# Kernel tuning notes

Hardware: AMD Instinct MI355X
Metric: run time of the kernel (lower is better)

## Reference

```python
import jax, jax.numpy as jnp
import numpy as np

B, C, H, W = 16, 256, 64, 64
K, HID, ITERS, EPS = 4, 512, 3, 1e-8


def _ln(x, g, b, eps=1e-5):
    m = jnp.mean(x, axis=-1, keepdims=True)
    v = jnp.mean((x - m) ** 2, axis=-1, keepdims=True)
    return (x - m) * jax.lax.rsqrt(v + eps) * g + b


def setup_inputs() -> dict:
    key = jax.random.key(0)
    ks = jax.random.split(key, 24)

    def lin(k, o, i):
        lim = np.sqrt(6.0 / (o + i)).astype(np.float32)
        return jax.random.uniform(k, (o, i), jnp.float32, -lim, lim)

    return {
        "x": jax.random.normal(ks[0], (B, C, H, W), jnp.float32),
        "noise": jax.random.normal(ks[1], (B, K, C), jnp.float32),
        "slot_mu": jax.random.normal(ks[2], (1, 1, C), jnp.float32),
        "slot_log_sigma": jnp.zeros((1, 1, C), jnp.float32),
        "ln_in_g": jnp.ones((C,)), "ln_in_b": jnp.zeros((C,)),
        "ln_sl_g": jnp.ones((C,)), "ln_sl_b": jnp.zeros((C,)),
        "ln_mlp_g": jnp.ones((C,)), "ln_mlp_b": jnp.zeros((C,)),
        "Wq": lin(ks[3], C, C), "bq": jnp.zeros((C,)),
        "Wk": lin(ks[4], C, C), "bk": jnp.zeros((C,)),
        "Wv": lin(ks[5], C, C), "bv": jnp.zeros((C,)),
        "Wu": lin(ks[6], C, 2 * C), "bu": jnp.zeros((C,)),
        "W1": lin(ks[7], HID, C), "b1": jnp.zeros((HID,)),
        "W2": lin(ks[8], C, HID), "b2": jnp.zeros((C,)),
        "We1": lin(ks[9], C // 2, C), "be1": jnp.zeros((C // 2,)),
        "We2": lin(ks[10], 1, C // 2), "be2": jnp.zeros((1,)),
    }


def reference(x, noise, slot_mu, slot_log_sigma, ln_in_g, ln_in_b, ln_sl_g, ln_sl_b,
              ln_mlp_g, ln_mlp_b, Wq, bq, Wk, bk, Wv, bv, Wu, bu, W1, b1, W2, b2,
              We1, be1, We2, be2):
    # b c h w -> b (h w) c
    xn = x.reshape(B, C, H * W).transpose(0, 2, 1)
    xn = _ln(xn, ln_in_g, ln_in_b)
    # k, v depend only on xn; hoisted out of the loop (same math)
    k = jnp.einsum('bnc,dc->bnd', xn, Wk) + bk
    v = jnp.einsum('bnc,dc->bnd', xn, Wv) + bv
    scale = C ** (-0.5)
    slots = slot_mu + jnp.exp(slot_log_sigma) * noise
    for _ in range(ITERS):
        prev = slots
        s = _ln(slots, ln_sl_g, ln_sl_b)
        q = jnp.einsum('bkc,dc->bkd', s, Wq) + bq
        attn = jax.nn.softmax(jnp.einsum('bkc,bnc->bkn', q, k) * scale, axis=1)
        w = attn / (jnp.sum(attn, axis=-1, keepdims=True) + EPS)
        updates = jnp.einsum('bkn,bnc->bkc', w, v)
        combined = jnp.concatenate([prev, updates], axis=-1)  # (B,K,2C)
        slots = jnp.einsum('bkc,dc->bkd', combined, Wu) + bu + prev
        m = _ln(slots, ln_mlp_g, ln_mlp_b)
        h = jax.nn.gelu(jnp.einsum('bkc,hc->bkh', m, W1) + b1, approximate=False)
        slots = slots + jnp.einsum('bkh,ch->bkc', h, W2) + b2
    e = jax.nn.gelu(jnp.einsum('bkc,dc->bkd', slots, We1) + be1, approximate=False)
    slot_weights = jax.nn.sigmoid(jnp.einsum('bkd,od->bko', e, We2) + be2)[..., 0]
    return slots, slot_weights
```

## Files before the change

### kernel.cpp

```cpp
#include <hip/hip_runtime.h>
#include <math.h>

#define B_    16
#define C_    256
#define NPIX  4096
#define K_    4
#define HID_  512
#define ITERS_ 3
#define NROWS (B_*NPIX)
#define EPS_  1e-8f

__device__ __forceinline__ float gelu_f(float x) {
    return 0.5f * x * (1.0f + erff(x * 0.70710678118654752f));
}

__device__ __forceinline__ unsigned short f2bf(float x) {
    union { float f; unsigned u; } v; v.f = x;
    unsigned r = v.u + 0x7fffu + ((v.u >> 16) & 1u);
    return (unsigned short)(r >> 16);
}
__device__ __forceinline__ float bflo(unsigned u) {
    union { unsigned u; float f; } v; v.u = u << 16; return v.f;
}
__device__ __forceinline__ float bfhi(unsigned u) {
    union { unsigned u; float f; } v; v.u = u & 0xffff0000u; return v.f;
}
__device__ __forceinline__ float4 shfl_xor4(float4 v, int m) {
    v.x = __shfl_xor(v.x, m); v.y = __shfl_xor(v.y, m);
    v.z = __shfl_xor(v.z, m); v.w = __shfl_xor(v.w, m);
    return v;
}
__device__ __forceinline__ void fma4(float4& a, const float4 w, const float4 s) {
    a.x = fmaf(w.x, s.x, a.x); a.y = fmaf(w.y, s.y, a.y);
    a.z = fmaf(w.z, s.z, a.z); a.w = fmaf(w.w, s.w, a.w);
}
__device__ __forceinline__ float hsum4(const float4 a) {
    return (a.x + a.y) + (a.z + a.w);
}

__device__ __forceinline__ void redpair256t(float a, float b, int t, float* r8,
                                            float& o1, float& o2) {
    #pragma unroll
    for (int m = 1; m <= 32; m <<= 1) { a += __shfl_xor(a, m); b += __shfl_xor(b, m); }
    if ((t & 63) == 0) { r8[(t >> 6) * 2] = a; r8[(t >> 6) * 2 + 1] = b; }
    __syncthreads();
    o1 = r8[0] + r8[2] + r8[4] + r8[6];
    o2 = r8[1] + r8[3] + r8[5] + r8[7];
}

__global__ __launch_bounds__(256) void prep_pack_kernel(
    const float* __restrict__ Wu, const float* __restrict__ W1,
    const float* __restrict__ W2, const float* __restrict__ We1,
    const float* __restrict__ Wq, const float* __restrict__ bk,
    const float* __restrict__ bq,
    float4* __restrict__ WuC4, float4* __restrict__ W14,
    float4* __restrict__ W24, float4* __restrict__ We14,
    float* __restrict__ wqoff) {
    __shared__ float r4[4];
    int i = blockIdx.x * 256 + threadIdx.x;
    if (blockIdx.x == 352) {
        int c = threadIdx.x;
        float s = 0.f;
        for (int dd = 0; dd < 256; ++dd) s = fmaf(Wq[dd * 256 + c], bk[dd], s);
        wqoff[c] = s;
        float p = bq[c] * bk[c];
        #pragma unroll
        for (int m = 1; m <= 32; m <<= 1) p += __shfl_xor(p, m);
        if ((c & 63) == 0) r4[c >> 6] = p;
        __syncthreads();
        if (c == 0) wqoff[256] = r4[0] + r4[1] + r4[2] + r4[3];
        return;
    }
    if (i < 16384) {
        int c4 = i >> 8, dd = i & 255;
        WuC4[i] = *(const float4*)&Wu[dd * 512 + c4 * 4];
    } else if (i < 49152) {
        int j = i - 16384; int c4 = j >> 9, h = j & 511;
        W14[j] = *(const float4*)&W1[h * 256 + c4 * 4];
    } else if (i < 81920) {
        int j = i - 49152; int h4 = j >> 8, dd = j & 255;
        W24[j] = *(const float4*)&W2[dd * 512 + h4 * 4];
    } else {
        int j = i - 81920; int c4 = j >> 7, e = j & 127;
        We14[j] = *(const float4*)&We1[e * 256 + c4 * 4];
    }
}

__global__ __launch_bounds__(256) void prep_compose_kernel(
    const float* __restrict__ Wu, const float* __restrict__ Wv,
    const float* __restrict__ Wk, const float* __restrict__ Wq,
    const float* __restrict__ bv, const float* __restrict__ bq,
    float4* __restrict__ WuC4, float4* __restrict__ Wqk4,
    float* __restrict__ bv2, float* __restrict__ bqk) {
    __shared__ float wur[256], wkc[256];
    __shared__ float ldsA[256], ldsB[256];
    __shared__ float r1[4], r2[4];
    const int d = blockIdx.x, c = threadIdx.x;
    wur[c] = Wu[d * 512 + 256 + c];
    wkc[c] = Wk[c * 256 + d];
    __syncthreads();
    float a = 0.f, b = 0.f;
    #pragma unroll 4
    for (int e = 0; e < 256; ++e) {
        a = fmaf(wur[e], Wv[e * 256 + c], a);
        b = fmaf(wkc[e], Wq[e * 256 + c], b);
    }
    ldsA[c] = a; ldsB[c] = b;
    float p1 = wur[c] * bv[c], p2 = wkc[c] * bq[c];
    #pragma unroll
    for (int m = 1; m <= 32; m <<= 1) { p1 += __shfl_xor(p1, m); p2 += __shfl_xor(p2, m); }
    if ((c & 63) == 0) { r1[c >> 6] = p1; r2[c >> 6] = p2; }
    __syncthreads();
    if (c < 64) {
        float4 qa = { ldsA[4 * c], ldsA[4 * c + 1], ldsA[4 * c + 2], ldsA[4 * c + 3] };
        float4 qb = { ldsB[4 * c], ldsB[4 * c + 1], ldsB[4 * c + 2], ldsB[4 * c + 3] };
        WuC4[(64 + c) * 256 + d] = qa;
        Wqk4[c * 256 + d] = qb;
    }
    if (c == 0) {
        bv2[d] = r1[0] + r1[1] + r1[2] + r1[3];
        bqk[d] = r2[0] + r2[1] + r2[2] + r2[3];
    }
}

__global__ __launch_bounds__(256) void xn_fused_kernel(
    const float* __restrict__ x, const float* __restrict__ g, const float* __restrict__ bta,
    unsigned short* __restrict__ xnb) {
    __shared__ float tile[256][65];
    __shared__ float sg[256], sb[256];
    __shared__ float red1[256], red2[256];
    __shared__ float smean[64], srstd[64];
    const int tid = threadIdx.x;
    const int nt = blockIdx.x << 6, b = blockIdx.y;

    sg[tid] = g[tid]; sb[tid] = bta[tid];
    #pragma unroll
    for (int r = 0; r < 64; ++r) {
        int idx = tid + (r << 8);
        int c_l = idx >> 6, n_l = idx & 63;
        tile[c_l][n_l] = x[(size_t)(b * C_ + c_l) * NPIX + nt + n_l];
    }
    __syncthreads();
    {
        int cq = tid >> 6, n_l = tid & 63;
        float s = 0.f, s2 = 0.f;
        #pragma unroll 8
        for (int c = cq * 64; c < cq * 64 + 64; ++c) {
            float v = tile[c][n_l];
            s += v; s2 += v * v;
        }
        red1[tid] = s; red2[tid] = s2;
    }
    __syncthreads();
    if (tid < 64) {
        float s  = red1[tid] + red1[tid + 64] + red1[tid + 128] + red1[tid + 192];
        float s2 = red2[tid] + red2[tid + 64] + red2[tid + 128] + red2[tid + 192];
        float m = s * (1.0f / C_);
        smean[tid] = m;
        srstd[tid] = rsqrtf(s2 * (1.0f / C_) - m * m + 1e-5f);
    }
    __syncthreads();
    #pragma unroll
    for (int r = 0; r < 32; ++r) {
        int idx = tid + (r << 8);
        int n_l = idx >> 7, cp = idx & 127;
        int c0 = cp << 1;
        float mn = smean[n_l], rs = srstd[n_l];
        float v0 = (tile[c0][n_l] - mn) * rs * sg[c0] + sb[c0];
        float v1 = (tile[c0 + 1][n_l] - mn) * rs * sg[c0 + 1] + sb[c0 + 1];
        ushort2 o; o.x = f2bf(v0); o.y = f2bf(v1);
        *reinterpret_cast<ushort2*>(&xnb[((size_t)(b * NPIX + nt + n_l)) * C_ + c0]) = o;
    }
}


__global__ __launch_bounds__(256) void init_slots_kernel(
    const float* __restrict__ noise, const float* __restrict__ mu,
    const float* __restrict__ log_sigma,
    float* __restrict__ slots, float* __restrict__ usum, float* __restrict__ denom) {
    int t = threadIdx.x, r = blockIdx.x;
    float v = mu[t] + expf(log_sigma[t]) * noise[r * C_ + t];
    slots[r * C_ + t] = v;
    usum[r * C_ + t] = 0.f;
    if (t == 0) denom[r] = 0.f;
}

__global__ __launch_bounds__(256) void qt_kernel(
    const float* __restrict__ src,
    const float* __restrict__ g_sl, const float* __restrict__ b_sl,
    const float4* __restrict__ Wqk4, const float* __restrict__ bqk,
    const float* __restrict__ wqoff,
    float* __restrict__ qtbuf, float* __restrict__ qoffbuf) {
    __shared__ __align__(16) float snorm[256];
    __shared__ float pq[256];
    __shared__ float r8[8];
    const int t = threadIdx.x, dq = blockIdx.x, r = blockIdx.y;
    float v = src[r * C_ + t];
    float sm, s2;
    redpair256t(v, v * v, t, r8, sm, s2);
    float mean = sm * (1.f / C_);
    float rs = rsqrtf(s2 * (1.f / C_) - mean * mean + 1e-5f);
    snorm[t] = (v - mean) * rs * g_sl[t] + b_sl[t];
    __syncthreads();
    const float4* sn4 = (const float4*)snorm;
    const int dloc = t & 63, ks = t >> 6;
    const int d = dq * 64 + dloc;
    {
        float4 a0 = {0,0,0,0}, a1 = {0,0,0,0};
        int c4b = ks << 4;
        #pragma unroll
        for (int i = 0; i < 16; i += 2) {
            fma4(a0, Wqk4[(c4b + i) * 256 + d], sn4[c4b + i]);
            fma4(a1, Wqk4[(c4b + i + 1) * 256 + d], sn4[c4b + i + 1]);
        }
        pq[ks * 64 + dloc] = hsum4(a0) + hsum4(a1);
    }
    __syncthreads();
    if (t < 64) {
        float s = pq[t] + pq[64 + t] + pq[128 + t] + pq[192 + t];
        qtbuf[r * C_ + dq * 64 + t] = s + bqk[dq * 64 + t];
    }
    if (dq == 0) {
        float p = snorm[t] * wqoff[t];
        #pragma unroll
        for (int m = 1; m <= 32; m <<= 1) p += __shfl_xor(p, m);
        if ((t & 63) == 0) r8[t >> 6] = p;
        __syncthreads();
        if (t == 0) qoffbuf[r] = r8[0] + r8[1] + r8[2] + r8[3] + wqoff[256];
    }
}

__global__ __launch_bounds__(256) void upd_wu_kernel(
    const float* __restrict__ slots, const float* __restrict__ usum,
    const float* __restrict__ denom,
    const float4* __restrict__ WuC4, const float* __restrict__ bu,
    const float* __restrict__ bv2,
    float* __restrict__ nvbuf) {
    __shared__ __align__(16) float comb[512];
    __shared__ float pq[256];
    __shared__ float sden, sscale;
    const int t = threadIdx.x, dq = blockIdx.x, r = blockIdx.y;
    if (t == 0) { float dv = denom[r]; sden = dv + EPS_; sscale = dv / (dv + EPS_); }
    comb[t] = slots[r * C_ + t];
    float uv = usum[r * C_ + t];
    __syncthreads();
    comb[256 + t] = uv / sden;
    __syncthreads();
    const float4* cb4 = (const float4*)comb;
    const int dloc = t & 31, ks = t >> 5;
    const int d = dq * 32 + dloc;
    {
        float4 a0 = {0,0,0,0}, a1 = {0,0,0,0};
        int c4b = ks << 4;
        #pragma unroll
        for (int i = 0; i < 16; i += 2) {
            fma4(a0, WuC4[(c4b + i) * 256 + d], cb4[c4b + i]);
            fma4(a1, WuC4[(c4b + i + 1) * 256 + d], cb4[c4b + i + 1]);
        }
        pq[ks * 32 + dloc] = hsum4(a0) + hsum4(a1);
    }
    __syncthreads();
    if (t < 32) {
        int dd = dq * 32 + t;
        float s = 0.f;
        #pragma unroll
        for (int i = 0; i < 8; ++i) s += pq[i * 32 + t];
        nvbuf[r * C_ + dd] = s + bu[dd] + comb[dd] + sscale * bv2[dd];
    }
}

__global__ __launch_bounds__(256) void upd_w1_kernel(
    const float* __restrict__ nvbuf,
    const float* __restrict__ g_mlp, const float* __restrict__ b_mlp,
    const float4* __restrict__ W14, const float* __restrict__ b1,
    float* __restrict__ hbuf, float* __restrict__ usum, float* __restrict__ denom) {
    __shared__ __align__(16) float mrow[256];
    __shared__ float pq[256];
    __shared__ float r8[8];
    const int t = threadIdx.x, hq = blockIdx.x, r = blockIdx.y;
    float nv = nvbuf[r * C_ + t];
    float sm, s2;
    redpair256t(nv, nv * nv, t, r8, sm, s2);
    float mean = sm * (1.f / C_);
    float rs = rsqrtf(s2 * (1.f / C_) - mean * mean + 1e-5f);
    mrow[t] = (nv - mean) * rs * g_mlp[t] + b_mlp[t];
    if (hq == 0) {
        usum[r * C_ + t] = 0.f;
        if (t == 0) denom[r] = 0.f;
    }
    __syncthreads();
    const float4* m4 = (const float4*)mrow;
    const int hloc = t & 63, ks = t >> 6;
    const int h = hq * 64 + hloc;
    {
        float4 a0 = {0,0,0,0}, a1 = {0,0,0,0};
        int c4b = ks << 4;
        #pragma unroll
        for (int i = 0; i < 16; i += 2) {
            fma4(a0, W14[(c4b + i) * 512 + h], m4[c4b + i]);
            fma4(a1, W14[(c4b + i + 1) * 512 + h], m4[c4b + i + 1]);
        }
        pq[ks * 64 + hloc] = hsum4(a0) + hsum4(a1);
    }
    __syncthreads();
    if (t < 64) {
        float s = pq[t] + pq[64 + t] + pq[128 + t] + pq[192 + t];
        hbuf[r * HID_ + hq * 64 + t] = gelu_f(s + b1[hq * 64 + t]);
    }
}

__global__ __launch_bounds__(256) void upd_w2_kernel(
    const float* __restrict__ nvbuf, const float* __restrict__ hbuf,
    const float4* __restrict__ W24, const float* __restrict__ b2,
    float* __restrict__ dst) {
    __shared__ __align__(16) float hrow[512];
    __shared__ float pq[256];
    const int t = threadIdx.x, dq = blockIdx.x, r = blockIdx.y;
    hrow[t] = hbuf[r * HID_ + t];
    hrow[256 + t] = hbuf[r * HID_ + 256 + t];
    __syncthreads();
    const float4* h4 = (const float4*)hrow;
    const int dloc = t & 31, ks = t >> 5;
    const int d = dq * 32 + dloc;
    {
        float4 a0 = {0,0,0,0}, a1 = {0,0,0,0};
        int h4b = ks << 4;
        #pragma unroll
        for (int i = 0; i < 16; i += 2) {
            fma4(a0, W24[(h4b + i) * 256 + d], h4[h4b + i]);
            fma4(a1, W24[(h4b + i + 1) * 256 + d], h4[h4b + i + 1]);
        }
        pq[ks * 32 + dloc] = hsum4(a0) + hsum4(a1);
    }
    __syncthreads();
    if (t < 32) {
        int dd = dq * 32 + t;
        float s = 0.f;
        #pragma unroll
        for (int i = 0; i < 8; ++i) s += pq[i * 32 + t];
        dst[r * C_ + dd] = nvbuf[r * C_ + dd] + s + b2[dd];
    }
}

__global__ __launch_bounds__(256) void head_kernel(
    const float* __restrict__ ovbuf,
    const float4* __restrict__ We14, const float* __restrict__ be1,
    const float* __restrict__ We2, const float* __restrict__ be2,
    float* __restrict__ out) {
    __shared__ __align__(16) float mrow[256];
    __shared__ float pq[256];
    __shared__ float erow[128];
    __shared__ float r4[4];
    const int t = threadIdx.x, r = blockIdx.x;
    mrow[t] = ovbuf[r * C_ + t];
    __syncthreads();
    const float4* m4 = (const float4*)mrow;
    const int e = t & 127, o2 = t >> 7;
    {
        float4 a0 = {0,0,0,0}, a1 = {0,0,0,0};
        int c4b = o2 << 5;
        #pragma unroll
        for (int i = 0; i < 32; i += 2) {
            fma4(a0, We14[(c4b + i) * 128 + e], m4[c4b + i]);
            fma4(a1, We14[(c4b + i + 1) * 128 + e], m4[c4b + i + 1]);
        }
        pq[o2 * 128 + e] = hsum4(a0) + hsum4(a1);
    }
    __syncthreads();
    if (t < 128) erow[t] = gelu_f(pq[t] + pq[128 + t] + be1[t]);
    __syncthreads();
    if (t < 64) {
        float p = We2[t] * erow[t] + We2[t + 64] * erow[t + 64];
        #pragma unroll
        for (int m = 1; m <= 32; m <<= 1) p += __shfl_xor(p, m);
        if (t == 0) { r4[0] = p; }
    }
    __syncthreads();
    if (t == 0) out[B_ * K_ * C_ + r] = 1.0f / (1.0f + expf(-(r4[0] + be2[0])));
}

__global__ __launch_bounds__(256) void attn_fused_kernel(
    const float* __restrict__ qtbuf, const float* __restrict__ qoffbuf,
    const unsigned short* __restrict__ xnb,
    float* __restrict__ usum, float* __restrict__ denom) {
    __shared__ float4 qT[264];
    __shared__ float attns[K_][64];
    __shared__ float upd_s[K_][256];
    __shared__ float asw[4][4];
    __shared__ float4 qo_s;

    const int tid = threadIdx.x;
    const int b = blockIdx.y;
    const int chunk = blockIdx.x;
    const int n0 = chunk << 6;
    const int wave = tid >> 6, lane = tid & 63;

    {
        int c = tid;
        float4 qv;
        qv.x = qtbuf[b * 1024 + c];
        qv.y = qtbuf[b * 1024 + 256 + c];
        qv.z = qtbuf[b * 1024 + 512 + c];
        qv.w = qtbuf[b * 1024 + 768 + c];
        qT[c + (c >> 5)] = qv;
        if (tid == 0) qo_s = *(const float4*)&qoffbuf[b * 4];
    }
    __syncthreads();

    const int cpart = tid & 7;
    const int npair = tid >> 3;
    const int c0 = cpart << 5;
    float4 acc0 = {0.f, 0.f, 0.f, 0.f}, acc1 = {0.f, 0.f, 0.f, 0.f};
    const unsigned short* kbase = xnb + ((size_t)b * NPIX + n0 + npair * 2) * C_ + c0;
    #pragma unroll
    for (int j = 0; j < 4; ++j) {
        uint4 k0 = *reinterpret_cast<const uint4*>(kbase + j * 8);
        uint4 k1 = *reinterpret_cast<const uint4*>(kbase + C_ + j * 8);
        const unsigned kw0[4] = {k0.x, k0.y, k0.z, k0.w};
        const unsigned kw1[4] = {k1.x, k1.y, k1.z, k1.w};
        #pragma unroll
        for (int jj = 0; jj < 4; ++jj) {
            int cidx = c0 + j * 8 + jj * 2 + cpart;
            float4 qa = qT[cidx];
            float4 qb = qT[cidx + 1];
            float f00 = bflo(kw0[jj]), f01 = bfhi(kw0[jj]);
            float f10 = bflo(kw1[jj]), f11 = bfhi(kw1[jj]);
            acc0.x += f00 * qa.x + f01 * qb.x;  acc0.y += f00 * qa.y + f01 * qb.y;
            acc0.z += f00 * qa.z + f01 * qb.z;  acc0.w += f00 * qa.w + f01 * qb.w;
            acc1.x += f10 * qa.x + f11 * qb.x;  acc1.y += f10 * qa.y + f11 * qb.y;
            acc1.z += f10 * qa.z + f11 * qb.z;  acc1.w += f10 * qa.w + f11 * qb.w;
        }
    }
    #pragma unroll
    for (int m = 1; m <= 4; m <<= 1) {
        acc0 = acc0 + shfl_xor4(acc0, m);
        acc1 = acc1 + shfl_xor4(acc1, m);
    }
    float4 w0, w1;
    {
        float4 l = (acc0 + qo_s) * 0.0625f;
        float mx = fmaxf(fmaxf(l.x, l.y), fmaxf(l.z, l.w));
        w0.x = expf(l.x - mx); w0.y = expf(l.y - mx);
        w0.z = expf(l.z - mx); w0.w = expf(l.w - mx);
        float inv = 1.0f / (w0.x + w0.y + w0.z + w0.w);
        w0 = w0 * inv;
        l = (acc1 + qo_s) * 0.0625f;
        mx = fmaxf(fmaxf(l.x, l.y), fmaxf(l.z, l.w));
        w1.x = expf(l.x - mx); w1.y = expf(l.y - mx);
        w1.z = expf(l.z - mx); w1.w = expf(l.w - mx);
        inv = 1.0f / (w1.x + w1.y + w1.z + w1.w);
        w1 = w1 * inv;
    }
    if (cpart == 0) {
        int n_l = npair * 2;
        attns[0][n_l] = w0.x; attns[1][n_l] = w0.y; attns[2][n_l] = w0.z; attns[3][n_l] = w0.w;
        attns[0][n_l + 1] = w1.x; attns[1][n_l + 1] = w1.y;
        attns[2][n_l + 1] = w1.z; attns[3][n_l + 1] = w1.w;
    }
    float4 ws = w0 + w1;
    #pragma unroll
    for (int m = 8; m <= 32; m <<= 1) ws = ws + shfl_xor4(ws, m);
    if (lane == 0) {
        asw[wave][0] = ws.x; asw[wave][1] = ws.y; asw[wave][2] = ws.z; asw[wave][3] = ws.w;
    }
    __syncthreads();
    if (tid < 4)
        atomicAdd(&denom[b * 4 + tid],
                  asw[0][tid] + asw[1][tid] + asw[2][tid] + asw[3][tid]);

    const int h = wave >> 1;
    const int chalf = (wave & 1) << 7;
    const int c = chalf + lane * 2;
    float a0[K_] = {0.f, 0.f, 0.f, 0.f};
    float a1[K_] = {0.f, 0.f, 0.f, 0.f};
    const unsigned short* vbase = xnb + ((size_t)b * NPIX + n0 + h * 32) * C_ + c;
    #pragma unroll 4
    for (int nn = 0; nn < 32; ++nn) {
        unsigned vv = *reinterpret_cast<const unsigned*>(vbase + (size_t)nn * C_);
        float v0 = bflo(vv), v1 = bfhi(vv);
        int n_l = h * 32 + nn;
        float q0 = attns[0][n_l], q1 = attns[1][n_l], q2 = attns[2][n_l], q3 = attns[3][n_l];
        a0[0] = fmaf(q0, v0, a0[0]); a1[0] = fmaf(q0, v1, a1[0]);
        a0[1] = fmaf(q1, v0, a0[1]); a1[1] = fmaf(q1, v1, a1[1]);
        a0[2] = fmaf(q2, v0, a0[2]); a1[2] = fmaf(q2, v1, a1[2]);
        a0[3] = fmaf(q3, v0, a0[3]); a1[3] = fmaf(q3, v1, a1[3]);
    }
    __syncthreads();
    if (h == 0) {
        #pragma unroll
        for (int k = 0; k < K_; ++k) { upd_s[k][c] = a0[k]; upd_s[k][c + 1] = a1[k]; }
    }
    __syncthreads();
    if (h == 1) {
        #pragma unroll
        for (int k = 0; k < K_; ++k) { upd_s[k][c] += a0[k]; upd_s[k][c + 1] += a1[k]; }
    }
    __syncthreads();
    #pragma unroll
    for (int k = 0; k < K_; ++k)
        atomicAdd(&usum[((size_t)b * K_ + k) * 256 + tid], upd_s[k][tid]);
}

extern "C" void kernel_launch(void* const* d_in, const int* in_sizes, int n_in,
                              void* d_out, int out_size, void* d_ws, size_t ws_size,
                              hipStream_t stream) {
    (void)in_sizes; (void)n_in; (void)out_size; (void)ws_size;
    const float* x        = (const float*)d_in[0];
    const float* noise    = (const float*)d_in[1];
    const float* slot_mu  = (const float*)d_in[2];
    const float* slot_ls  = (const float*)d_in[3];
    const float* ln_in_g  = (const float*)d_in[4];
    const float* ln_in_b  = (const float*)d_in[5];
    const float* ln_sl_g  = (const float*)d_in[6];
    const float* ln_sl_b  = (const float*)d_in[7];
    const float* ln_mlp_g = (const float*)d_in[8];
    const float* ln_mlp_b = (const float*)d_in[9];
    const float* Wq = (const float*)d_in[10];
    const float* bq = (const float*)d_in[11];
    const float* Wk = (const float*)d_in[12];
    const float* bk = (const float*)d_in[13];
    const float* Wv = (const float*)d_in[14];
    const float* bv = (const float*)d_in[15];
    const float* Wu = (const float*)d_in[16];
    const float* bu = (const float*)d_in[17];
    const float* W1 = (const float*)d_in[18];
    const float* b1 = (const float*)d_in[19];
    const float* W2 = (const float*)d_in[20];
    const float* b2 = (const float*)d_in[21];
    const float* We1 = (const float*)d_in[22];
    const float* be1 = (const float*)d_in[23];
    const float* We2 = (const float*)d_in[24];
    const float* be2 = (const float*)d_in[25];
    float* out = (float*)d_out;

    char* ws = (char*)d_ws;
    unsigned short* xnb = (unsigned short*)ws;
    float4* WuC4 = (float4*)(xnb + (size_t)NROWS * C_);
    float4* W14  = WuC4 + 32768;
    float4* W24  = W14 + 32768;
    float4* We14 = W24 + 32768;
    float4* Wqk4 = We14 + 8192;
    float* bv2   = (float*)(Wqk4 + 16384);
    float* bqk   = bv2 + 256;
    float* wqoff = bqk + 256;
    float* slots = wqoff + 260;
    float* qtbuf = slots + B_ * K_ * C_;
    float* qoffb = qtbuf + B_ * K_ * C_;
    float* usum  = qoffb + B_ * K_;
    float* denom = usum + B_ * K_ * C_;
    float* nvbuf = denom + B_ * K_;
    float* hbuf  = nvbuf + B_ * K_ * C_;

    prep_pack_kernel<<<353, 256, 0, stream>>>(Wu, W1, W2, We1, Wq, bk, bq,
                                              WuC4, W14, W24, We14, wqoff);
    prep_compose_kernel<<<256, 256, 0, stream>>>(Wu, Wv, Wk, Wq, bv, bq,
                                                 WuC4, Wqk4, bv2, bqk);
    xn_fused_kernel<<<dim3(64, 16), 256, 0, stream>>>(x, ln_in_g, ln_in_b, xnb);
    init_slots_kernel<<<B_ * K_, 256, 0, stream>>>(noise, slot_mu, slot_ls,
                                                   slots, usum, denom);
    qt_kernel<<<dim3(4, B_ * K_), 256, 0, stream>>>(slots, ln_sl_g, ln_sl_b,
                                                    Wqk4, bqk, wqoff, qtbuf, qoffb);
    for (int it = 0; it < ITERS_; ++it) {
        attn_fused_kernel<<<dim3(64, 16), 256, 0, stream>>>(qtbuf, qoffb, xnb,
                                                            usum, denom);
        upd_wu_kernel<<<dim3(8, B_ * K_), 256, 0, stream>>>(slots, usum, denom,
                                                            WuC4, bu, bv2, nvbuf);
        upd_w1_kernel<<<dim3(8, B_ * K_), 256, 0, stream>>>(nvbuf, ln_mlp_g, ln_mlp_b,
                                                            W14, b1, hbuf, usum, denom);
        upd_w2_kernel<<<dim3(8, B_ * K_), 256, 0, stream>>>(
            nvbuf, hbuf, W24, b2, (it < ITERS_ - 1) ? slots : out);
        if (it < ITERS_ - 1)
            qt_kernel<<<dim3(4, B_ * K_), 256, 0, stream>>>(slots, ln_sl_g, ln_sl_b,
                                                            Wqk4, bqk, wqoff, qtbuf, qoffb);
    }
    head_kernel<<<B_ * K_, 256, 0, stream>>>(out, We14, be1, We2, be2, out);
}
```

Before: 299.0 us.

## Fold layer norms into precomposed weights and fuse per-iteration slot kernels

Layer-norm gamma/beta for the slot and MLP norms are folded into transposed weight matrices plus precomputed row sums. Each norm can then be applied after the matvec from per-row mean and square-sum statistics gathered with atomics. This collapses the per-iteration chain (Wu, W1, W2 and the q projection) from four kernels into two. It also merges the prep kernels into one and moves the head's first layer into the update. The input layernorm kernel is widened to 512 threads with statistics gathered during the load. The aim is fewer launches and serial dependencies, at the cost of atomic accumulation, zeroing handoffs between kernels, and E[x²]-mean² numerics.

```diff
diff --git a/kernel.cpp b/kernel.cpp
--- a/kernel.cpp
+++ b/kernel.cpp
@@ -38,131 +38,160 @@
     return (a.x + a.y) + (a.z + a.w);
 }
 
-__device__ __forceinline__ void redpair256t(float a, float b, int t, float* r8,
-                                            float& o1, float& o2) {
-    #pragma unroll
-    for (int m = 1; m <= 32; m <<= 1) { a += __shfl_xor(a, m); b += __shfl_xor(b, m); }
-    if ((t & 63) == 0) { r8[(t >> 6) * 2] = a; r8[(t >> 6) * 2 + 1] = b; }
-    __syncthreads();
-    o1 = r8[0] + r8[2] + r8[4] + r8[6];
-    o2 = r8[1] + r8[3] + r8[5] + r8[7];
-}
-
-__global__ __launch_bounds__(256) void prep_pack_kernel(
+__global__ __launch_bounds__(256) void prep_all_kernel(
     const float* __restrict__ Wu, const float* __restrict__ W1,
     const float* __restrict__ W2, const float* __restrict__ We1,
-    const float* __restrict__ Wq, const float* __restrict__ bk,
-    const float* __restrict__ bq,
-    float4* __restrict__ WuC4, float4* __restrict__ W14,
-    float4* __restrict__ W24, float4* __restrict__ We14,
-    float* __restrict__ wqoff) {
-    __shared__ float r4[4];
-    int i = blockIdx.x * 256 + threadIdx.x;
-    if (blockIdx.x == 352) {
-        int c = threadIdx.x;
-        float s = 0.f;
-        for (int dd = 0; dd < 256; ++dd) s = fmaf(Wq[dd * 256 + c], bk[dd], s);
-        wqoff[c] = s;
-        float p = bq[c] * bk[c];
-        #pragma unroll
-        for (int m = 1; m <= 32; m <<= 1) p += __shfl_xor(p, m);
-        if ((c & 63) == 0) r4[c >> 6] = p;
-        __syncthreads();
-        if (c == 0) wqoff[256] = r4[0] + r4[1] + r4[2] + r4[3];
-        return;
-    }
-    if (i < 16384) {
+    const float* __restrict__ Wq, const float* __restrict__ Wk,
+    const float* __restrict__ Wv,
+    const float* __restrict__ bk, const float* __restrict__ bq,
+    const float* __restrict__ bv, const float* __restrict__ b1,
+    const float* __restrict__ g_sl, const float* __restrict__ b_sl,
+    const float* __restrict__ g_mlp, const float* __restrict__ b_mlp,
+    float4* __restrict__ WuC4, float4* __restrict__ W24,
+    float* __restrict__ W1gT, float* __restrict__ WqgT,
+    float* __restrict__ We1T,
+    float* __restrict__ w1gsum, float* __restrict__ w1bsum,
+    float* __restrict__ wqgsum, float* __restrict__ wqbsum,
+    float* __restrict__ wqg, float* __restrict__ wqS,
+    float* __restrict__ bv2) {
+    const int role = blockIdx.x;
+    const int t = threadIdx.x;
+    if (role < 64) {
+        int i = role * 256 + t;
         int c4 = i >> 8, dd = i & 255;
         WuC4[i] = *(const float4*)&Wu[dd * 512 + c4 * 4];
-    } else if (i < 49152) {
-        int j = i - 16384; int c4 = j >> 9, h = j & 511;
-        W14[j] = *(const float4*)&W1[h * 256 + c4 * 4];
-    } else if (i < 81920) {
-        int j = i - 49152; int h4 = j >> 8, dd = j & 255;
+        return;
+    }
+    if (role < 192) {
+        int j = (role - 64) * 256 + t;
+        int h4 = j >> 8, dd = j & 255;
         W24[j] = *(const float4*)&W2[dd * 512 + h4 * 4];
-    } else {
-        int j = i - 81920; int c4 = j >> 7, e = j & 127;
-        We14[j] = *(const float4*)&We1[e * 256 + c4 * 4];
-    }
-}
-
-__global__ __launch_bounds__(256) void prep_compose_kernel(
-    const float* __restrict__ Wu, const float* __restrict__ Wv,
-    const float* __restrict__ Wk, const float* __restrict__ Wq,
-    const float* __restrict__ bv, const float* __restrict__ bq,
-    float4* __restrict__ WuC4, float4* __restrict__ Wqk4,
-    float* __restrict__ bv2, float* __restrict__ bqk) {
-    __shared__ float wur[256], wkc[256];
-    __shared__ float ldsA[256], ldsB[256];
-    __shared__ float r1[4], r2[4];
-    const int d = blockIdx.x, c = threadIdx.x;
-    wur[c] = Wu[d * 512 + 256 + c];
-    wkc[c] = Wk[c * 256 + d];
-    __syncthreads();
-    float a = 0.f, b = 0.f;
-    #pragma unroll 4
-    for (int e = 0; e < 256; ++e) {
-        a = fmaf(wur[e], Wv[e * 256 + c], a);
-        b = fmaf(wkc[e], Wq[e * 256 + c], b);
-    }
-    ldsA[c] = a; ldsB[c] = b;
-    float p1 = wur[c] * bv[c], p2 = wkc[c] * bq[c];
-    #pragma unroll
-    for (int m = 1; m <= 32; m <<= 1) { p1 += __shfl_xor(p1, m); p2 += __shfl_xor(p2, m); }
-    if ((c & 63) == 0) { r1[c >> 6] = p1; r2[c >> 6] = p2; }
-    __syncthreads();
-    if (c < 64) {
-        float4 qa = { ldsA[4 * c], ldsA[4 * c + 1], ldsA[4 * c + 2], ldsA[4 * c + 3] };
-        float4 qb = { ldsB[4 * c], ldsB[4 * c + 1], ldsB[4 * c + 2], ldsB[4 * c + 3] };
-        WuC4[(64 + c) * 256 + d] = qa;
-        Wqk4[c * 256 + d] = qb;
-    }
-    if (c == 0) {
-        bv2[d] = r1[0] + r1[1] + r1[2] + r1[3];
-        bqk[d] = r2[0] + r2[1] + r2[2] + r2[3];
-    }
-}
-
-__global__ __launch_bounds__(256) void xn_fused_kernel(
+        return;
+    }
+    if (role < 704) {
+        int idx = (role - 192) * 256 + t;
+        int c = idx & 255, jj = idx >> 8;
+        W1gT[c * 512 + jj] = W1[jj * 256 + c] * g_mlp[c];
+        return;
+    }
+    if (role < 832) {
+        int idx = (role - 704) * 256 + t;
+        int c = idx & 255, e = idx >> 8;
+        We1T[c * 128 + e] = We1[e * 256 + c];
+        return;
+    }
+    if (role == 832) {
+        __shared__ float r12[12];
+        int c = t;
+        float w = 0.f;
+        for (int dd = 0; dd < 256; ++dd) w = fmaf(Wq[dd * 256 + c], bk[dd], w);
+        wqg[c] = w * g_sl[c];
+        float pA = w * g_sl[c], pB = w * b_sl[c], pC = bq[c] * bk[c];
+        #pragma unroll
+        for (int m = 1; m <= 32; m <<= 1) {
+            pA += __shfl_xor(pA, m); pB += __shfl_xor(pB, m); pC += __shfl_xor(pC, m);
+        }
+        if ((c & 63) == 0) {
+            int w4 = c >> 6;
+            r12[w4] = pA; r12[4 + w4] = pB; r12[8 + w4] = pC;
+        }
+        __syncthreads();
+        if (c == 0) {
+            wqS[0] = r12[0] + r12[1] + r12[2] + r12[3];
+            wqS[1] = (r12[4] + r12[5] + r12[6] + r12[7])
+                   + (r12[8] + r12[9] + r12[10] + r12[11]);
+        }
+        return;
+    }
+    if (role < 835) {
+        int j = (role - 833) * 256 + t;
+        float sg = 0.f, sb = 0.f;
+        for (int c = 0; c < 256; ++c) {
+            float w = W1[j * 256 + c];
+            sg = fmaf(w, g_mlp[c], sg);
+            sb = fmaf(w, b_mlp[c], sb);
+        }
+        w1gsum[j] = sg;
+        w1bsum[j] = sb + b1[j];
+        return;
+    }
+    {
+        __shared__ float wur[256], wkc[256];
+        __shared__ float ldsA[256];
+        __shared__ float r16[16];
+        const int d = role - 835, c = t;
+        wur[c] = Wu[d * 512 + 256 + c];
+        wkc[c] = Wk[c * 256 + d];
+        __syncthreads();
+        float a = 0.f, b = 0.f;
+        #pragma unroll 4
+        for (int e = 0; e < 256; ++e) {
+            a = fmaf(wur[e], Wv[e * 256 + c], a);
+            b = fmaf(wkc[e], Wq[e * 256 + c], b);
+        }
+        ldsA[c] = a;
+        WqgT[c * 256 + d] = b * g_sl[c];
+        float pA = wur[c] * bv[c];
+        float pB = wkc[c] * bq[c];
+        float pC = b * g_sl[c];
+        float pD = b * b_sl[c];
+        #pragma unroll
+        for (int m = 1; m <= 32; m <<= 1) {
+            pA += __shfl_xor(pA, m); pB += __shfl_xor(pB, m);
+            pC += __shfl_xor(pC, m); pD += __shfl_xor(pD, m);
+        }
+        if ((c & 63) == 0) {
+            int w4 = c >> 6;
+            r16[w4] = pA; r16[4 + w4] = pB; r16[8 + w4] = pC; r16[12 + w4] = pD;
+        }
+        __syncthreads();
+        if (c < 64) {
+            float4 qa = { ldsA[4 * c], ldsA[4 * c + 1], ldsA[4 * c + 2], ldsA[4 * c + 3] };
+            WuC4[(64 + c) * 256 + d] = qa;
+        }
+        if (c == 0) {
+            bv2[d] = r16[0] + r16[1] + r16[2] + r16[3];
+            float bqk = r16[4] + r16[5] + r16[6] + r16[7];
+            wqgsum[d] = r16[8] + r16[9] + r16[10] + r16[11];
+            wqbsum[d] = (r16[12] + r16[13] + r16[14] + r16[15]) + bqk;
+        }
+    }
+}
+
+__global__ __launch_bounds__(512) void xn_fused_kernel(
     const float* __restrict__ x, const float* __restrict__ g, const float* __restrict__ bta,
     unsigned short* __restrict__ xnb) {
     __shared__ float tile[256][65];
     __shared__ float sg[256], sb[256];
-    __shared__ float red1[256], red2[256];
+    __shared__ float red1[512], red2[512];
     __shared__ float smean[64], srstd[64];
     const int tid = threadIdx.x;
     const int nt = blockIdx.x << 6, b = blockIdx.y;
 
-    sg[tid] = g[tid]; sb[tid] = bta[tid];
-    #pragma unroll
-    for (int r = 0; r < 64; ++r) {
-        int idx = tid + (r << 8);
-        int c_l = idx >> 6, n_l = idx & 63;
-        tile[c_l][n_l] = x[(size_t)(b * C_ + c_l) * NPIX + nt + n_l];
-    }
-    __syncthreads();
-    {
-        int cq = tid >> 6, n_l = tid & 63;
-        float s = 0.f, s2 = 0.f;
-        #pragma unroll 8
-        for (int c = cq * 64; c < cq * 64 + 64; ++c) {
-            float v = tile[c][n_l];
-            s += v; s2 += v * v;
-        }
-        red1[tid] = s; red2[tid] = s2;
-    }
-    __syncthreads();
-    if (tid < 64) {
-        float s  = red1[tid] + red1[tid + 64] + red1[tid + 128] + red1[tid + 192];
-        float s2 = red2[tid] + red2[tid + 64] + red2[tid + 128] + red2[tid + 192];
-        float m = s * (1.0f / C_);
-        smean[tid] = m;
-        srstd[tid] = rsqrtf(s2 * (1.0f / C_) - m * m + 1e-5f);
-    }
-    __syncthreads();
+    if (tid < 256) { sg[tid] = g[tid]; sb[tid] = bta[tid]; }
+    float s = 0.f, s2 = 0.f;
     #pragma unroll
     for (int r = 0; r < 32; ++r) {
-        int idx = tid + (r << 8);
+        int idx = tid + (r << 9);
+        int c_l = idx >> 6, n_l = idx & 63;
+        float v = x[(size_t)(b * C_ + c_l) * NPIX + nt + n_l];
+        tile[c_l][n_l] = v;
+        s += v; s2 += v * v;
+    }
+    red1[tid] = s; red2[tid] = s2;
+    __syncthreads();
+    if (tid < 64) {
+        float a = 0.f, a2 = 0.f;
+        #pragma unroll
+        for (int j = 0; j < 8; ++j) { a += red1[tid + 64 * j]; a2 += red2[tid + 64 * j]; }
+        float m = a * (1.0f / C_);
+        smean[tid] = m;
+        srstd[tid] = rsqrtf(a2 * (1.0f / C_) - m * m + 1e-5f);
+    }
+    __syncthreads();
+    #pragma unroll
+    for (int r = 0; r < 16; ++r) {
+        int idx = tid + (r << 9);
         int n_l = idx >> 7, cp = idx & 127;
         int c0 = cp << 1;
         float mn = smean[n_l], rs = srstd[n_l];
@@ -173,83 +202,81 @@
     }
 }
 
-
-__global__ __launch_bounds__(256) void init_slots_kernel(
+__global__ __launch_bounds__(256) void initqt_kernel(
     const float* __restrict__ noise, const float* __restrict__ mu,
     const float* __restrict__ log_sigma,
-    float* __restrict__ slots, float* __restrict__ usum, float* __restrict__ denom) {
-    int t = threadIdx.x, r = blockIdx.x;
-    float v = mu[t] + expf(log_sigma[t]) * noise[r * C_ + t];
-    slots[r * C_ + t] = v;
-    usum[r * C_ + t] = 0.f;
-    if (t == 0) denom[r] = 0.f;
-}
-
-__global__ __launch_bounds__(256) void qt_kernel(
-    const float* __restrict__ src,
-    const float* __restrict__ g_sl, const float* __restrict__ b_sl,
-    const float4* __restrict__ Wqk4, const float* __restrict__ bqk,
-    const float* __restrict__ wqoff,
-    float* __restrict__ qtbuf, float* __restrict__ qoffbuf) {
-    __shared__ __align__(16) float snorm[256];
+    const float* __restrict__ WqgT, const float* __restrict__ wqg,
+    float* __restrict__ slots,
+    float* __restrict__ qtp, float* __restrict__ qoffP,
+    float* __restrict__ msumS, float* __restrict__ m2sumS,
+    float* __restrict__ usum, float* __restrict__ denom) {
+    __shared__ float srow[256];
     __shared__ float pq[256];
     __shared__ float r8[8];
     const int t = threadIdx.x, dq = blockIdx.x, r = blockIdx.y;
-    float v = src[r * C_ + t];
-    float sm, s2;
-    redpair256t(v, v * v, t, r8, sm, s2);
-    float mean = sm * (1.f / C_);
-    float rs = rsqrtf(s2 * (1.f / C_) - mean * mean + 1e-5f);
-    snorm[t] = (v - mean) * rs * g_sl[t] + b_sl[t];
-    __syncthreads();
-    const float4* sn4 = (const float4*)snorm;
-    const int dloc = t & 63, ks = t >> 6;
-    const int d = dq * 64 + dloc;
-    {
-        float4 a0 = {0,0,0,0}, a1 = {0,0,0,0};
-        int c4b = ks << 4;
-        #pragma unroll
-        for (int i = 0; i < 16; i += 2) {
-            fma4(a0, Wqk4[(c4b + i) * 256 + d], sn4[c4b + i]);
-            fma4(a1, Wqk4[(c4b + i + 1) * 256 + d], sn4[c4b + i + 1]);
-        }
-        pq[ks * 64 + dloc] = hsum4(a0) + hsum4(a1);
-    }
-    __syncthreads();
-    if (t < 64) {
-        float s = pq[t] + pq[64 + t] + pq[128 + t] + pq[192 + t];
-        qtbuf[r * C_ + dq * 64 + t] = s + bqk[dq * 64 + t];
-    }
+    float v = mu[t] + expf(log_sigma[t]) * noise[r * C_ + t];
+    srow[t] = v;
     if (dq == 0) {
-        float p = snorm[t] * wqoff[t];
-        #pragma unroll
-        for (int m = 1; m <= 32; m <<= 1) p += __shfl_xor(p, m);
-        if ((t & 63) == 0) r8[t >> 6] = p;
-        __syncthreads();
-        if (t == 0) qoffbuf[r] = r8[0] + r8[1] + r8[2] + r8[3] + wqoff[256];
-    }
-}
-
-__global__ __launch_bounds__(256) void upd_wu_kernel(
+        slots[r * C_ + t] = v;
+        usum[r * C_ + t] = 0.f;
+        if (t == 0) denom[r] = 0.f;
+        float a = v, b2s = v * v, c = wqg[t] * v;
+        #pragma unroll
+        for (int m = 1; m <= 32; m <<= 1) {
+            a += __shfl_xor(a, m); b2s += __shfl_xor(b2s, m); c += __shfl_xor(c, m);
+        }
+        if ((t & 63) == 0) {
+            int w4 = t >> 6;
+            r8[w4] = a; r8[4 + w4] = b2s;
+            pq[w4] = c;
+        }
+    }
+    __syncthreads();
+    if (dq == 0 && t == 0) {
+        msumS[r]  = r8[0] + r8[1] + r8[2] + r8[3];
+        m2sumS[r] = r8[4] + r8[5] + r8[6] + r8[7];
+        qoffP[r]  = pq[0] + pq[1] + pq[2] + pq[3];
+    }
+    __syncthreads();
+    const int dl = t & 127, cs = t >> 7;
+    const int d = dq * 128 + dl;
+    float acc = 0.f;
+    #pragma unroll 4
+    for (int c = cs * 128; c < cs * 128 + 128; ++c)
+        acc = fmaf(WqgT[c * 256 + d], srow[c], acc);
+    pq[cs * 128 + dl] = acc;
+    __syncthreads();
+    if (t < 128) qtp[r * C_ + dq * 128 + t] = pq[t] + pq[128 + t];
+}
+
+__global__ __launch_bounds__(256) void updA_kernel(
     const float* __restrict__ slots, const float* __restrict__ usum,
     const float* __restrict__ denom,
     const float4* __restrict__ WuC4, const float* __restrict__ bu,
-    const float* __restrict__ bv2,
-    float* __restrict__ nvbuf) {
+    const float* __restrict__ bv2, const float* __restrict__ W1gT,
+    float* __restrict__ nvbuf, float* __restrict__ hpp,
+    float* __restrict__ msumN, float* __restrict__ m2sumN,
+    float* __restrict__ qtp, float* __restrict__ qoffP,
+    float* __restrict__ msumS, float* __restrict__ m2sumS,
+    float* __restrict__ ep) {
     __shared__ __align__(16) float comb[512];
     __shared__ float pq[256];
+    __shared__ float nvs[32];
     __shared__ float sden, sscale;
     const int t = threadIdx.x, dq = blockIdx.x, r = blockIdx.y;
     if (t == 0) { float dv = denom[r]; sden = dv + EPS_; sscale = dv / (dv + EPS_); }
     comb[t] = slots[r * C_ + t];
     float uv = usum[r * C_ + t];
+    if (t < 32) qtp[r * C_ + dq * 32 + t] = 0.f;
+    if (dq < 4 && t < 32) ep[r * 128 + dq * 32 + t] = 0.f;
+    if (dq == 0 && t == 0) { msumS[r] = 0.f; m2sumS[r] = 0.f; qoffP[r] = 0.f; }
     __syncthreads();
     comb[256 + t] = uv / sden;
     __syncthreads();
-    const float4* cb4 = (const float4*)comb;
     const int dloc = t & 31, ks = t >> 5;
     const int d = dq * 32 + dloc;
     {
+        const float4* cb4 = (const float4*)comb;
         float4 a0 = {0,0,0,0}, a1 = {0,0,0,0};
         int c4b = ks << 4;
         #pragma unroll
@@ -265,64 +292,56 @@
         float s = 0.f;
         #pragma unroll
         for (int i = 0; i < 8; ++i) s += pq[i * 32 + t];
-        nvbuf[r * C_ + dd] = s + bu[dd] + comb[dd] + sscale * bv2[dd];
-    }
-}
-
-__global__ __launch_bounds__(256) void upd_w1_kernel(
-    const float* __restrict__ nvbuf,
-    const float* __restrict__ g_mlp, const float* __restrict__ b_mlp,
-    const float4* __restrict__ W14, const float* __restrict__ b1,
-    float* __restrict__ hbuf, float* __restrict__ usum, float* __restrict__ denom) {
-    __shared__ __align__(16) float mrow[256];
-    __shared__ float pq[256];
-    __shared__ float r8[8];
-    const int t = threadIdx.x, hq = blockIdx.x, r = blockIdx.y;
-    float nv = nvbuf[r * C_ + t];
-    float sm, s2;
-    redpair256t(nv, nv * nv, t, r8, sm, s2);
-    float mean = sm * (1.f / C_);
-    float rs = rsqrtf(s2 * (1.f / C_) - mean * mean + 1e-5f);
-    mrow[t] = (nv - mean) * rs * g_mlp[t] + b_mlp[t];
-    if (hq == 0) {
-        usum[r * C_ + t] = 0.f;
-        if (t == 0) denom[r] = 0.f;
-    }
-    __syncthreads();
-    const float4* m4 = (const float4*)mrow;
-    const int hloc = t & 63, ks = t >> 6;
-    const int h = hq * 64 + hloc;
+        float nv = s + bu[dd] + comb[dd] + sscale * bv2[dd];
+        nvs[t] = nv;
+        nvbuf[r * C_ + dd] = nv;
+        float a = nv, b = nv * nv;
+        #pragma unroll
+        for (int m = 1; m <= 16; m <<= 1) { a += __shfl_xor(a, m); b += __shfl_xor(b, m); }
+        if (t == 0) { atomicAdd(&msumN[r], a); atomicAdd(&m2sumN[r], b); }
+    }
+    __syncthreads();
     {
-        float4 a0 = {0,0,0,0}, a1 = {0,0,0,0};
-        int c4b = ks << 4;
-        #pragma unroll
-        for (int i = 0; i < 16; i += 2) {
-            fma4(a0, W14[(c4b + i) * 512 + h], m4[c4b + i]);
-            fma4(a1, W14[(c4b + i + 1) * 512 + h], m4[c4b + i + 1]);
-        }
-        pq[ks * 64 + hloc] = hsum4(a0) + hsum4(a1);
-    }
-    __syncthreads();
-    if (t < 64) {
-        float s = pq[t] + pq[64 + t] + pq[128 + t] + pq[192 + t];
-        hbuf[r * HID_ + hq * 64 + t] = gelu_f(s + b1[hq * 64 + t]);
-    }
-}
-
-__global__ __launch_bounds__(256) void upd_w2_kernel(
-    const float* __restrict__ nvbuf, const float* __restrict__ hbuf,
+        float a0 = 0.f, a1 = 0.f;
+        const float* wb = W1gT + (size_t)(dq * 32) * 512;
+        #pragma unroll 8
+        for (int i = 0; i < 32; ++i) {
+            float nv = nvs[i];
+            a0 = fmaf(wb[i * 512 + t], nv, a0);
+            a1 = fmaf(wb[i * 512 + 256 + t], nv, a1);
+        }
+        atomicAdd(&hpp[r * HID_ + t], a0);
+        atomicAdd(&hpp[r * HID_ + 256 + t], a1);
+    }
+}
+
+__global__ __launch_bounds__(256) void updB_kernel(
+    const float* __restrict__ nvbuf, const float* __restrict__ hpp,
+    const float* __restrict__ msumN, const float* __restrict__ m2sumN,
+    const float* __restrict__ w1gsum, const float* __restrict__ w1bsum,
     const float4* __restrict__ W24, const float* __restrict__ b2,
-    float* __restrict__ dst) {
+    const float* __restrict__ WqgT, const float* __restrict__ wqg,
+    const float* __restrict__ We1T,
+    float* __restrict__ dst,
+    float* __restrict__ qtp, float* __restrict__ qoffP,
+    float* __restrict__ msumS, float* __restrict__ m2sumS,
+    float* __restrict__ ep,
+    float* __restrict__ usum, float* __restrict__ denom, int fin) {
     __shared__ __align__(16) float hrow[512];
     __shared__ float pq[256];
+    __shared__ float ovs[32];
     const int t = threadIdx.x, dq = blockIdx.x, r = blockIdx.y;
-    hrow[t] = hbuf[r * HID_ + t];
-    hrow[256 + t] = hbuf[r * HID_ + 256 + t];
-    __syncthreads();
-    const float4* h4 = (const float4*)hrow;
+    float mN = msumN[r] * (1.f / C_);
+    float rsN = rsqrtf(m2sumN[r] * (1.f / C_) - mN * mN + 1e-5f);
+    hrow[t]       = gelu_f(rsN * (hpp[r * HID_ + t]       - mN * w1gsum[t])       + w1bsum[t]);
+    hrow[256 + t] = gelu_f(rsN * (hpp[r * HID_ + 256 + t] - mN * w1gsum[256 + t]) + w1bsum[256 + t]);
+    if (t < 32) usum[r * C_ + dq * 32 + t] = 0.f;
+    if (dq == 0 && t == 0) denom[r] = 0.f;
+    __syncthreads();
     const int dloc = t & 31, ks = t >> 5;
     const int d = dq * 32 + dloc;
     {
+        const float4* h4 = (const float4*)hrow;
         float4 a0 = {0,0,0,0}, a1 = {0,0,0,0};
         int h4b = ks << 4;
         #pragma unroll
@@ -338,56 +357,68 @@
         float s = 0.f;
         #pragma unroll
         for (int i = 0; i < 8; ++i) s += pq[i * 32 + t];
-        dst[r * C_ + dd] = nvbuf[r * C_ + dd] + s + b2[dd];
-    }
-}
-
-__global__ __launch_bounds__(256) void head_kernel(
-    const float* __restrict__ ovbuf,
-    const float4* __restrict__ We14, const float* __restrict__ be1,
+        float ov = nvbuf[r * C_ + dd] + s + b2[dd];
+        ovs[t] = ov;
+        dst[r * C_ + dd] = ov;
+        float a = ov, b = ov * ov;
+        #pragma unroll
+        for (int m = 1; m <= 16; m <<= 1) { a += __shfl_xor(a, m); b += __shfl_xor(b, m); }
+        if (t == 0) { atomicAdd(&msumS[r], a); atomicAdd(&m2sumS[r], b); }
+    }
+    __syncthreads();
+    if (!fin) {
+        float acc = 0.f;
+        const float* wb = WqgT + (size_t)(dq * 32) * 256;
+        #pragma unroll 8
+        for (int i = 0; i < 32; ++i)
+            acc = fmaf(wb[i * 256 + t], ovs[i], acc);
+        atomicAdd(&qtp[r * C_ + t], acc);
+        if (t < 32) {
+            float p = wqg[dq * 32 + t] * ovs[t];
+            #pragma unroll
+            for (int m = 1; m <= 16; m <<= 1) p += __shfl_xor(p, m);
+            if (t == 0) atomicAdd(&qoffP[r], p);
+        }
+    } else {
+        const int e = t & 127, half = t >> 7;
+        float acc = 0.f;
+        const float* wb = We1T + (size_t)(dq * 32 + half * 16) * 128;
+        #pragma unroll
+        for (int i = 0; i < 16; ++i)
+            acc = fmaf(wb[i * 128 + e], ovs[half * 16 + i], acc);
+        atomicAdd(&ep[r * 128 + e], acc);
+    }
+}
+
+__global__ __launch_bounds__(128) void head_fin_kernel(
+    const float* __restrict__ ep, const float* __restrict__ be1,
     const float* __restrict__ We2, const float* __restrict__ be2,
     float* __restrict__ out) {
-    __shared__ __align__(16) float mrow[256];
-    __shared__ float pq[256];
-    __shared__ float erow[128];
-    __shared__ float r4[4];
+    __shared__ float r2[2];
     const int t = threadIdx.x, r = blockIdx.x;
-    mrow[t] = ovbuf[r * C_ + t];
-    __syncthreads();
-    const float4* m4 = (const float4*)mrow;
-    const int e = t & 127, o2 = t >> 7;
-    {
-        float4 a0 = {0,0,0,0}, a1 = {0,0,0,0};
-        int c4b = o2 << 5;
-        #pragma unroll
-        for (int i = 0; i < 32; i += 2) {
-            fma4(a0, We14[(c4b + i) * 128 + e], m4[c4b + i]);
-            fma4(a1, We14[(c4b + i + 1) * 128 + e], m4[c4b + i + 1]);
-        }
-        pq[o2 * 128 + e] = hsum4(a0) + hsum4(a1);
-    }
-    __syncthreads();
-    if (t < 128) erow[t] = gelu_f(pq[t] + pq[128 + t] + be1[t]);
-    __syncthreads();
-    if (t < 64) {
-        float p = We2[t] * erow[t] + We2[t + 64] * erow[t + 64];
-        #pragma unroll
-        for (int m = 1; m <= 32; m <<= 1) p += __shfl_xor(p, m);
-        if (t == 0) { r4[0] = p; }
-    }
-    __syncthreads();
-    if (t == 0) out[B_ * K_ * C_ + r] = 1.0f / (1.0f + expf(-(r4[0] + be2[0])));
+    float ev = gelu_f(ep[r * 128 + t] + be1[t]);
+    float p = We2[t] * ev;
+    #pragma unroll
+    for (int m = 1; m <= 32; m <<= 1) p += __shfl_xor(p, m);
+    if ((t & 63) == 0) r2[t >> 6] = p;
+    __syncthreads();
+    if (t == 0) out[B_ * K_ * C_ + r] = 1.0f / (1.0f + expf(-(r2[0] + r2[1] + be2[0])));
 }
 
 __global__ __launch_bounds__(256) void attn_fused_kernel(
-    const float* __restrict__ qtbuf, const float* __restrict__ qoffbuf,
+    const float* __restrict__ qtp, const float* __restrict__ qoffP,
+    const float* __restrict__ msumS, const float* __restrict__ m2sumS,
+    const float* __restrict__ wqgsum, const float* __restrict__ wqbsum,
+    const float* __restrict__ wqS,
     const unsigned short* __restrict__ xnb,
-    float* __restrict__ usum, float* __restrict__ denom) {
+    float* __restrict__ usum, float* __restrict__ denom,
+    float* __restrict__ hpp, float* __restrict__ msumN, float* __restrict__ m2sumN) {
     __shared__ float4 qT[264];
     __shared__ float attns[K_][64];
     __shared__ float upd_s[K_][256];
     __shared__ float asw[4][4];
     __shared__ float4 qo_s;
+    __shared__ float s_m[4], s_rs[4];
 
     const int tid = threadIdx.x;
     const int b = blockIdx.y;
@@ -395,15 +426,36 @@
     const int n0 = chunk << 6;
     const int wave = tid >> 6, lane = tid & 63;
 
+    if (tid < 4) {
+        float ms = msumS[b * 4 + tid] * (1.f / C_);
+        float m2 = m2sumS[b * 4 + tid] * (1.f / C_);
+        s_m[tid] = ms;
+        s_rs[tid] = rsqrtf(m2 - ms * ms + 1e-5f);
+    }
+    if (chunk < 8) hpp[(size_t)(b * 4 + (chunk >> 1)) * HID_ + (chunk & 1) * 256 + tid] = 0.f;
+    else if (chunk == 8) {
+        if (tid < 4) msumN[b * 4 + tid] = 0.f;
+        else if (tid < 8) m2sumN[b * 4 + tid - 4] = 0.f;
+    }
+    __syncthreads();
     {
         int c = tid;
+        float wg = wqgsum[c], wb = wqbsum[c];
         float4 qv;
-        qv.x = qtbuf[b * 1024 + c];
-        qv.y = qtbuf[b * 1024 + 256 + c];
-        qv.z = qtbuf[b * 1024 + 512 + c];
-        qv.w = qtbuf[b * 1024 + 768 + c];
+        qv.x = s_rs[0] * (qtp[(b * 4 + 0) * C_ + c] - s_m[0] * wg) + wb;
+        qv.y = s_rs[1] * (qtp[(b * 4 + 1) * C_ + c] - s_m[1] * wg) + wb;
+        qv.z = s_rs[2] * (qtp[(b * 4 + 2) * C_ + c] - s_m[2] * wg) + wb;
+        qv.w = s_rs[3] * (qtp[(b * 4 + 3) * C_ + c] - s_m[3] * wg) + wb;
         qT[c + (c >> 5)] = qv;
-        if (tid == 0) qo_s = *(const float4*)&qoffbuf[b * 4];
+        if (tid == 0) {
+            float S1 = wqS[0], S2 = wqS[1];
+            float4 qo;
+            qo.x = s_rs[0] * (qoffP[b * 4 + 0] - s_m[0] * S1) + S2;
+            qo.y = s_rs[1] * (qoffP[b * 4 + 1] - s_m[1] * S1) + S2;
+            qo.z = s_rs[2] * (qoffP[b * 4 + 2] - s_m[2] * S1) + S2;
+            qo.w = s_rs[3] * (qoffP[b * 4 + 3] - s_m[3] * S1) + S2;
+            qo_s = qo;
+        }
     }
     __syncthreads();
 
@@ -535,43 +587,52 @@
 
     char* ws = (char*)d_ws;
     unsigned short* xnb = (unsigned short*)ws;
-    float4* WuC4 = (float4*)(xnb + (size_t)NROWS * C_);
-    float4* W14  = WuC4 + 32768;
-    float4* W24  = W14 + 32768;
-    float4* We14 = W24 + 32768;
-    float4* Wqk4 = We14 + 8192;
-    float* bv2   = (float*)(Wqk4 + 16384);
-    float* bqk   = bv2 + 256;
-    float* wqoff = bqk + 256;
-    float* slots = wqoff + 260;
-    float* qtbuf = slots + B_ * K_ * C_;
-    float* qoffb = qtbuf + B_ * K_ * C_;
-    float* usum  = qoffb + B_ * K_;
-    float* denom = usum + B_ * K_ * C_;
-    float* nvbuf = denom + B_ * K_;
-    float* hbuf  = nvbuf + B_ * K_ * C_;
-
-    prep_pack_kernel<<<353, 256, 0, stream>>>(Wu, W1, W2, We1, Wq, bk, bq,
-                                              WuC4, W14, W24, We14, wqoff);
-    prep_compose_kernel<<<256, 256, 0, stream>>>(Wu, Wv, Wk, Wq, bv, bq,
-                                                 WuC4, Wqk4, bv2, bqk);
-    xn_fused_kernel<<<dim3(64, 16), 256, 0, stream>>>(x, ln_in_g, ln_in_b, xnb);
-    init_slots_kernel<<<B_ * K_, 256, 0, stream>>>(noise, slot_mu, slot_ls,
-                                                   slots, usum, denom);
-    qt_kernel<<<dim3(4, B_ * K_), 256, 0, stream>>>(slots, ln_sl_g, ln_sl_b,
-                                                    Wqk4, bqk, wqoff, qtbuf, qoffb);
+    float4* WuC4  = (float4*)(xnb + (size_t)NROWS * C_);
+    float4* W24   = WuC4 + 32768;
+    float* W1gT   = (float*)(W24 + 32768);
+    float* WqgT   = W1gT + 131072;
+    float* We1T   = WqgT + 65536;
+    float* w1gsum = We1T + 32768;
+    float* w1bsum = w1gsum + 512;
+    float* wqgsum = w1bsum + 512;
+    float* wqbsum = wqgsum + 256;
+    float* wqg    = wqbsum + 256;
+    float* wqS    = wqg + 256;
+    float* bv2    = wqS + 4;
+    float* slots  = bv2 + 256;
+    float* nvbuf  = slots + B_ * K_ * C_;
+    float* qtp    = nvbuf + B_ * K_ * C_;
+    float* qoffP  = qtp + B_ * K_ * C_;
+    float* msumS  = qoffP + B_ * K_;
+    float* m2sumS = msumS + B_ * K_;
+    float* hpp    = m2sumS + B_ * K_;
+    float* msumN  = hpp + B_ * K_ * HID_;
+    float* m2sumN = msumN + B_ * K_;
+    float* usum   = m2sumN + B_ * K_;
+    float* denom  = usum + B_ * K_ * C_;
+    float* ep     = denom + B_ * K_;
+
+    prep_all_kernel<<<1091, 256, 0, stream>>>(
+        Wu, W1, W2, We1, Wq, Wk, Wv, bk, bq, bv, b1,
+        ln_sl_g, ln_sl_b, ln_mlp_g, ln_mlp_b,
+        WuC4, W24, W1gT, WqgT, We1T,
+        w1gsum, w1bsum, wqgsum, wqbsum, wqg, wqS, bv2);
+    xn_fused_kernel<<<dim3(64, 16), 512, 0, stream>>>(x, ln_in_g, ln_in_b, xnb);
+    initqt_kernel<<<dim3(2, B_ * K_), 256, 0, stream>>>(
+        noise, slot_mu, slot_ls, WqgT, wqg,
+        slots, qtp, qoffP, msumS, m2sumS, usum, denom);
     for (int it = 0; it < ITERS_; ++it) {
-        attn_fused_kernel<<<dim3(64, 16), 256, 0, stream>>>(qtbuf, qoffb, xnb,
-                                                            usum, denom);
-        upd_wu_kernel<<<dim3(8, B_ * K_), 256, 0, stream>>>(slots, usum, denom,
-                                                            WuC4, bu, bv2, nvbuf);
-        upd_w1_kernel<<<dim3(8, B_ * K_), 256, 0, stream>>>(nvbuf, ln_mlp_g, ln_mlp_b,
-                                                            W14, b1, hbuf, usum, denom);
-        upd_w2_kernel<<<dim3(8, B_ * K_), 256, 0, stream>>>(
-            nvbuf, hbuf, W24, b2, (it < ITERS_ - 1) ? slots : out);
-        if (it < ITERS_ - 1)
-            qt_kernel<<<dim3(4, B_ * K_), 256, 0, stream>>>(slots, ln_sl_g, ln_sl_b,
-                                                            Wqk4, bqk, wqoff, qtbuf, qoffb);
-    }
-    head_kernel<<<B_ * K_, 256, 0, stream>>>(out, We14, be1, We2, be2, out);
-}
+        const int fin = (it == ITERS_ - 1);
+        attn_fused_kernel<<<dim3(64, 16), 256, 0, stream>>>(
+            qtp, qoffP, msumS, m2sumS, wqgsum, wqbsum, wqS,
+            xnb, usum, denom, hpp, msumN, m2sumN);
+        updA_kernel<<<dim3(8, B_ * K_), 256, 0, stream>>>(
+            slots, usum, denom, WuC4, bu, bv2, W1gT,
+            nvbuf, hpp, msumN, m2sumN, qtp, qoffP, msumS, m2sumS, ep);
+        updB_kernel<<<dim3(8, B_ * K_), 256, 0, stream>>>(
+            nvbuf, hpp, msumN, m2sumN, w1gsum, w1bsum, W24, b2,
+            WqgT, wqg, We1T, fin ? out : slots,
+            qtp, qoffP, msumS, m2sumS, ep, usum, denom, fin);
+    }
+    head_fin_kernel<<<B_ * K_, 128, 0, stream>>>(ep, be1, We2, be2, out);
+}
```

Result: no change. 301.5 us (+0.8%).
